# Kernel tuning notes

Measured on AMD Instinct MI355X. Metric: run time of the kernel, lower is better.

## Reference

```python
import jax, jax.numpy as jnp
import numpy as np

DIM = 1024
HEADS = 8
DK = 64
DV = 64
B = 4
N = 2048
SCALE = DK ** -0.5


def setup_inputs() -> dict:
    key = jax.random.key(0)
    ks = jax.random.split(key, 6)
    x = jax.random.normal(ks[0], (B, N, DIM), dtype=jnp.float32)
    # xavier-uniform-like init scale for weights (stored as [in, out], i.e. W^T of torch Linear weight)
    def xavier(k, fan_in, fan_out):
        limit = (6.0 / (fan_in + fan_out)) ** 0.5
        return jax.random.uniform(k, (fan_in, fan_out), minval=-limit, maxval=limit, dtype=jnp.float32)
    Wq = xavier(ks[1], DIM, HEADS * DK)
    Wk = xavier(ks[2], DIM, HEADS * DK)
    Wv = xavier(ks[3], DIM, HEADS * DV)
    Wo = xavier(ks[4], HEADS * DV, DIM)
    bo = jnp.zeros((DIM,), dtype=jnp.float32)
    return {"x": x, "Wq": Wq, "Wk": Wk, "Wv": Wv, "Wo": Wo, "bo": bo}


def reference(x, Wq, Wk, Wv, Wo, bo):
    b, n, _ = x.shape
    # project and split heads: b n (h d) -> b h n d
    def split_heads(t, d):
        return t.reshape(b, n, HEADS, d).transpose(0, 2, 1, 3)
    q = split_heads(x @ Wq, DK) * SCALE
    k = split_heads(x @ Wk, DK)
    v = split_heads(x @ Wv, DV)
    logits = jnp.einsum('bhid,bhjd->bhij', q, k)  # [b,h,n,n]
    attn = jax.nn.softmax(logits, axis=-1)
    out = jnp.einsum('bhij,bhjd->bhid', attn, v)  # [b,h,n,dv]
    out = out.transpose(0, 2, 1, 3).reshape(b, n, HEADS * DV)
    return (out @ Wo + bo, attn)
```

## Files before the change

### kernel.cpp

```cpp
#include <hip/hip_runtime.h>
#include <stdint.h>

#define B_ 4
#define N_ 2048
#define H_ 8
#define BH_ 32
#define DIM_ 1024

typedef unsigned short ushort_t;
typedef float f32x4 __attribute__((ext_vector_type(4)));
typedef short bf16x8 __attribute__((ext_vector_type(8)));

__device__ __forceinline__ ushort_t f2bf(float f) {
  uint32_t u = __float_as_uint(f);
  u += 0x7fff + ((u >> 16) & 1);
  return (ushort_t)(u >> 16);
}

__device__ __forceinline__ void lds_load16(const void* g, void* l) {
  __builtin_amdgcn_global_load_lds(
      (const __attribute__((address_space(1))) unsigned int*)g,
      (__attribute__((address_space(3))) unsigned int*)l, 16, 0, 0);
}

__global__ void cvt_x_kernel(const float* __restrict__ src, ushort_t* __restrict__ dst) {
  int i = (blockIdx.x * 256 + threadIdx.x) * 4;
  float4 v = *(const float4*)(src + i);
  ushort4 o;
  o.x = f2bf(v.x); o.y = f2bf(v.y); o.z = f2bf(v.z); o.w = f2bf(v.w);
  *(ushort4*)(dst + i) = o;
}

__global__ void twT_kernel(const float* __restrict__ src, ushort_t* __restrict__ dst,
                           int R, int C) {
  __shared__ float t[32][33];
  int c0 = blockIdx.x * 32, r0 = blockIdx.y * 32;
  int tx = threadIdx.x, ty = threadIdx.y;
#pragma unroll
  for (int i = 0; i < 4; i++)
    t[ty + i * 8][tx] = src[(size_t)(r0 + ty + i * 8) * C + c0 + tx];
  __syncthreads();
#pragma unroll
  for (int i = 0; i < 4; i++)
    dst[(size_t)(c0 + ty + i * 8) * R + r0 + tx] = f2bf(t[tx][ty + i * 8]);
}

__global__ void tv_kernel(const ushort_t* __restrict__ V, ushort_t* __restrict__ Vt) {
  __shared__ ushort_t t[64][65];
  int bh = blockIdx.y, n0 = blockIdx.x * 64;
  int tid = threadIdx.x;
  const ushort_t* Vh = V + (size_t)bh * N_ * 64;
  ushort_t* Vth = Vt + (size_t)bh * 64 * N_;
#pragma unroll
  for (int i = 0; i < 16; i++) {
    int idx = tid + i * 256;
    int r = idx >> 6, c = idx & 63;
    t[r][c] = Vh[(size_t)(n0 + r) * 64 + c];
  }
  __syncthreads();
#pragma unroll
  for (int i = 0; i < 16; i++) {
    int idx = tid + i * 256;
    int d = idx >> 6, c = idx & 63;
    Vth[(size_t)d * N_ + n0 + c] = t[c][d];
  }
}

template <int MODE>
__global__ __launch_bounds__(256)
void gemm_bf16_kernel(const ushort_t* __restrict__ A, const ushort_t* __restrict__ BT,
                      int K, int Ncols,
                      ushort_t* __restrict__ qb, ushort_t* __restrict__ kb2,
                      ushort_t* __restrict__ vb,
                      float* __restrict__ outp, const float* __restrict__ bias) {
  __shared__ ushort_t As[128 * 32];
  __shared__ ushort_t Bs[128 * 32];
  const int n0 = blockIdx.x * 128, m0 = blockIdx.y * 128;
  const int tid = threadIdx.x;
  const int lane = tid & 63, wave = tid >> 6;
  const int quad = lane >> 4, l16 = lane & 15;
  const int wm = (wave >> 1) * 64, wn = (wave & 1) * 64;
  f32x4 acc[4][4] = {};
  const int arow = tid >> 2, achk = tid & 3;
  const ushort_t* Ag = A + (size_t)(m0 + arow) * K + achk * 8;
  const ushort_t* Bg = BT + (size_t)(n0 + arow) * K + achk * 8;
  ushort_t* asd = As + tid * 8;
  ushort_t* bsd = Bs + tid * 8;
  const int nk = K >> 5;
  for (int ks = 0; ks < nk; ks++) {
    __syncthreads();
    lds_load16(Ag + ks * 32, asd);
    lds_load16(Ag + (size_t)64 * K + ks * 32, asd + 64 * 32);
    lds_load16(Bg + ks * 32, bsd);
    lds_load16(Bg + (size_t)64 * K + ks * 32, bsd + 64 * 32);
    __syncthreads();
    bf16x8 af[4], bfr[4];
#pragma unroll
    for (int i = 0; i < 4; i++)
      af[i] = *(const bf16x8*)(As + (wm + i * 16 + l16) * 32 + quad * 8);
#pragma unroll
    for (int i = 0; i < 4; i++)
      bfr[i] = *(const bf16x8*)(Bs + (wn + i * 16 + l16) * 32 + quad * 8);
#pragma unroll
    for (int i = 0; i < 4; i++)
#pragma unroll
      for (int j = 0; j < 4; j++)
        acc[i][j] = __builtin_amdgcn_mfma_f32_16x16x32_bf16(af[i], bfr[j], acc[i][j], 0, 0, 0);
  }
#pragma unroll
  for (int i = 0; i < 4; i++)
#pragma unroll
    for (int j = 0; j < 4; j++)
#pragma unroll
      for (int r = 0; r < 4; r++) {
        int gm = m0 + wm + i * 16 + quad * 4 + r;
        int gn = n0 + wn + j * 16 + l16;
        float v = acc[i][j][r];
        if (MODE == 0) {
          int b = gm >> 11, n = gm & (N_ - 1);
          int part = gn >> 9;
          int cc = gn & 511;
          int h = cc >> 6, d = cc & 63;
          size_t dst = ((size_t)(b * H_ + h) * N_ + n) * 64 + d;
          if (part == 0) qb[dst] = f2bf(v * 0.125f);
          else if (part == 1) kb2[dst] = f2bf(v);
          else vb[dst] = f2bf(v);
        } else {
          outp[(size_t)gm * Ncols + gn] = v + bias[gn];
        }
      }
}

#define PCOLS 1032
__global__ __launch_bounds__(512, 4)
void attn_kernel(const ushort_t* __restrict__ Q, const ushort_t* __restrict__ Kb,
                 const ushort_t* __restrict__ Vt, float* __restrict__ attn_out,
                 ushort_t* __restrict__ Ob) {
  __shared__ ushort_t Pl[16 * PCOLS];
  __shared__ float redA[8 * 16];
  __shared__ float redB[8 * 16];
  __shared__ float Ored[4 * 256];
  const int bh = blockIdx.y;
  const int q0 = blockIdx.x * 16;
  const int tid = threadIdx.x;
  const int w = tid >> 6, lane = tid & 63, quad = lane >> 4, l16 = lane & 15;

  const ushort_t* Qh = Q + (size_t)bh * N_ * 64;
  const ushort_t* Kh = Kb + (size_t)bh * N_ * 64;
  const ushort_t* Vh = Vt + (size_t)bh * 64 * N_;

  bf16x8 qf0 = *(const bf16x8*)(Qh + (size_t)(q0 + l16) * 64 + quad * 8);
  bf16x8 qf1 = *(const bf16x8*)(Qh + (size_t)(q0 + l16) * 64 + 32 + quad * 8);

  const int ncol0 = w * 256;
  f32x4 acc[16];
#pragma unroll
  for (int t = 0; t < 16; t++) {
    const ushort_t* kp = Kh + (size_t)(ncol0 + t * 16 + l16) * 64 + quad * 8;
    bf16x8 kf0 = *(const bf16x8*)kp;
    bf16x8 kf1 = *(const bf16x8*)(kp + 32);
    f32x4 z = {};
    z = __builtin_amdgcn_mfma_f32_16x16x32_bf16(qf0, kf0, z, 0, 0, 0);
    acc[t] = __builtin_amdgcn_mfma_f32_16x16x32_bf16(qf1, kf1, z, 0, 0, 0);
  }

  float mx[4];
#pragma unroll
  for (int r = 0; r < 4; r++) {
    float m = acc[0][r];
#pragma unroll
    for (int t = 1; t < 16; t++) m = fmaxf(m, acc[t][r]);
    for (int off = 1; off < 16; off <<= 1) m = fmaxf(m, __shfl_xor(m, off));
    mx[r] = m;
  }
  if (l16 == 0)
#pragma unroll
    for (int r = 0; r < 4; r++) redA[w * 16 + quad * 4 + r] = mx[r];
  __syncthreads();
#pragma unroll
  for (int r = 0; r < 4; r++) {
    float m = redA[quad * 4 + r];
#pragma unroll
    for (int ww = 1; ww < 8; ww++) m = fmaxf(m, redA[ww * 16 + quad * 4 + r]);
    mx[r] = m;
  }

  float sm[4] = {0.f, 0.f, 0.f, 0.f};
#pragma unroll
  for (int t = 0; t < 16; t++)
#pragma unroll
    for (int r = 0; r < 4; r++) {
      float p = __expf(acc[t][r] - mx[r]);
      acc[t][r] = p;
      sm[r] += p;
    }
#pragma unroll
  for (int r = 0; r < 4; r++) {
    float s = sm[r];
    for (int off = 1; off < 16; off <<= 1) s += __shfl_xor(s, off);
    sm[r] = s;
  }
  if (l16 == 0)
#pragma unroll
    for (int r = 0; r < 4; r++) redB[w * 16 + quad * 4 + r] = sm[r];
  __syncthreads();
  float inv[4];
#pragma unroll
  for (int r = 0; r < 4; r++) {
    float s = 0.f;
#pragma unroll
    for (int ww = 0; ww < 8; ww++) s += redB[ww * 16 + quad * 4 + r];
    inv[r] = 1.0f / s;
  }
#pragma unroll
  for (int t = 0; t < 16; t++)
#pragma unroll
    for (int r = 0; r < 4; r++) acc[t][r] *= inv[r];

  float* ar = attn_out + ((size_t)bh * N_ + q0) * N_;
#pragma unroll
  for (int t = 0; t < 16; t++) {
    int col = ncol0 + t * 16 + l16;
#pragma unroll
    for (int r = 0; r < 4; r++)
      ar[(size_t)(quad * 4 + r) * N_ + col] = acc[t][r];
  }

  const int jt = w & 3, kh = w >> 2;
  f32x4 oacc = {};
  for (int ph = 0; ph < 2; ph++) {
    if (kh == ph) {
#pragma unroll
      for (int t = 0; t < 16; t++) {
        int colb = jt * 256 + t * 16 + l16;
#pragma unroll
        for (int r = 0; r < 4; r++)
          Pl[(quad * 4 + r) * PCOLS + colb] = f2bf(acc[t][r]);
      }
    }
    __syncthreads();
#pragma unroll
    for (int s = 0; s < 16; s++) {
      int klocal = kh * 512 + s * 32;
      bf16x8 pf = *(const bf16x8*)(Pl + l16 * PCOLS + klocal + quad * 8);
      const ushort_t* vp = Vh + (size_t)(jt * 16 + l16) * N_ + ph * 1024 + klocal + quad * 8;
      bf16x8 vf = *(const bf16x8*)vp;
      oacc = __builtin_amdgcn_mfma_f32_16x16x32_bf16(pf, vf, oacc, 0, 0, 0);
    }
    __syncthreads();
  }
  if (w >= 4) {
#pragma unroll
    for (int r = 0; r < 4; r++)
      Ored[jt * 256 + (quad * 4 + r) * 16 + l16] = oacc[r];
  }
  __syncthreads();
  if (w < 4) {
    int b = bh >> 3, h = bh & 7;
#pragma unroll
    for (int r = 0; r < 4; r++) {
      float s = oacc[r] + Ored[jt * 256 + (quad * 4 + r) * 16 + l16];
      Ob[((size_t)(b * N_ + q0 + quad * 4 + r)) * 512 + h * 64 + jt * 16 + l16] = f2bf(s);
    }
  }
}

extern "C" void kernel_launch(void* const* d_in, const int* in_sizes, int n_in,
                              void* d_out, int out_size, void* d_ws, size_t ws_size,
                              hipStream_t stream) {
  const float* x  = (const float*)d_in[0];
  const float* Wq = (const float*)d_in[1];
  const float* Wk = (const float*)d_in[2];
  const float* Wv = (const float*)d_in[3];
  const float* Wo = (const float*)d_in[4];
  const float* bo = (const float*)d_in[5];
  float* outp = (float*)d_out;
  float* attnp = outp + (size_t)B_ * N_ * DIM_;

  char* ws = (char*)d_ws;
  ushort_t* xbf   = (ushort_t*)(ws);
  ushort_t* WallT = (ushort_t*)(ws + 16777216);
  ushort_t* WoT   = (ushort_t*)(ws + 19922944);
  ushort_t* Qb    = (ushort_t*)(ws + 20971520);
  ushort_t* Kb    = (ushort_t*)(ws + 29360128);
  ushort_t* Vb    = (ushort_t*)(ws + 37748736);
  ushort_t* Vt    = (ushort_t*)(ws + 46137344);
  ushort_t* Ob    = (ushort_t*)(ws + 54525952);

  cvt_x_kernel<<<dim3(8192), dim3(256), 0, stream>>>(x, xbf);
  twT_kernel<<<dim3(16, 32), dim3(32, 8), 0, stream>>>(Wq, WallT, 1024, 512);
  twT_kernel<<<dim3(16, 32), dim3(32, 8), 0, stream>>>(Wk, WallT + 512 * 1024, 1024, 512);
  twT_kernel<<<dim3(16, 32), dim3(32, 8), 0, stream>>>(Wv, WallT + 1024 * 1024, 1024, 512);
  twT_kernel<<<dim3(32, 16), dim3(32, 8), 0, stream>>>(Wo, WoT, 512, 1024);

  gemm_bf16_kernel<0><<<dim3(12, 64), dim3(256), 0, stream>>>(
      xbf, WallT, 1024, 1536, Qb, Kb, Vb, nullptr, nullptr);

  tv_kernel<<<dim3(32, 32), dim3(256), 0, stream>>>(Vb, Vt);

  attn_kernel<<<dim3(128, 32), dim3(512), 0, stream>>>(Qb, Kb, Vt, attnp, Ob);

  gemm_bf16_kernel<1><<<dim3(8, 64), dim3(256), 0, stream>>>(
      Ob, WoT, 512, 1024, nullptr, nullptr, nullptr, outp, bo);
}
```

Before: 875.5 us.

## Remap block order for XCD locality, merge weight transposes, use nontemporal stores

Flattens the grids of the projection GEMMs and the attention kernel and remaps block indices so that consecutive blocks landing on the same XCD (round-robin over 8) process neighbouring tiles or the same head. This improves L2 reuse of K/V and of the GEMM operands. The large fp32 attention-matrix store and the output-projection store become nontemporal, so the streaming writes pollute the cache less. The three QKV weight-transpose launches are merged into one 3D-grid launch to cut launch overhead.

```diff
diff --git a/kernel.cpp b/kernel.cpp
--- a/kernel.cpp
+++ b/kernel.cpp
@@ -43,6 +43,22 @@
 #pragma unroll
   for (int i = 0; i < 4; i++)
     dst[(size_t)(c0 + ty + i * 8) * R + r0 + tx] = f2bf(t[tx][ty + i * 8]);
+}
+
+__global__ void twT3_kernel(const float* __restrict__ Wq, const float* __restrict__ Wk,
+                            const float* __restrict__ Wv, ushort_t* __restrict__ dst) {
+  __shared__ float t[32][33];
+  const float* src = (blockIdx.z == 0) ? Wq : (blockIdx.z == 1) ? Wk : Wv;
+  ushort_t* d = dst + (size_t)blockIdx.z * 512 * 1024;
+  int c0 = blockIdx.x * 32, r0 = blockIdx.y * 32;
+  int tx = threadIdx.x, ty = threadIdx.y;
+#pragma unroll
+  for (int i = 0; i < 4; i++)
+    t[ty + i * 8][tx] = src[(size_t)(r0 + ty + i * 8) * 512 + c0 + tx];
+  __syncthreads();
+#pragma unroll
+  for (int i = 0; i < 4; i++)
+    d[(size_t)(c0 + ty + i * 8) * 1024 + r0 + tx] = f2bf(t[tx][ty + i * 8]);
 }
 
 __global__ void tv_kernel(const ushort_t* __restrict__ V, ushort_t* __restrict__ Vt) {
@@ -75,7 +91,12 @@
                       float* __restrict__ outp, const float* __restrict__ bias) {
   __shared__ ushort_t As[128 * 32];
   __shared__ ushort_t Bs[128 * 32];
-  const int n0 = blockIdx.x * 128, m0 = blockIdx.y * 128;
+  const int cpx = (int)gridDim.x >> 3;
+  const int flat = blockIdx.x;
+  const int orig = (flat & 7) * cpx + (flat >> 3);
+  const int nbx = (MODE == 0) ? 12 : 8;
+  const int bx = orig % nbx, by = orig / nbx;
+  const int n0 = bx * 128, m0 = by * 128;
   const int tid = threadIdx.x;
   const int lane = tid & 63, wave = tid >> 6;
   const int quad = lane >> 4, l16 = lane & 15;
@@ -126,7 +147,7 @@
           else if (part == 1) kb2[dst] = f2bf(v);
           else vb[dst] = f2bf(v);
         } else {
-          outp[(size_t)gm * Ncols + gn] = v + bias[gn];
+          __builtin_nontemporal_store(v + bias[gn], &outp[(size_t)gm * Ncols + gn]);
         }
       }
 }
@@ -140,8 +161,10 @@
   __shared__ float redA[8 * 16];
   __shared__ float redB[8 * 16];
   __shared__ float Ored[4 * 256];
-  const int bh = blockIdx.y;
-  const int q0 = blockIdx.x * 16;
+  const int flat = blockIdx.x;
+  const int orig = (flat & 7) * 512 + (flat >> 3);
+  const int bh = orig >> 7;
+  const int q0 = (orig & 127) * 16;
   const int tid = threadIdx.x;
   const int w = tid >> 6, lane = tid & 63, quad = lane >> 4, l16 = lane & 15;
 
@@ -223,7 +246,7 @@
     int col = ncol0 + t * 16 + l16;
 #pragma unroll
     for (int r = 0; r < 4; r++)
-      ar[(size_t)(quad * 4 + r) * N_ + col] = acc[t][r];
+      __builtin_nontemporal_store(acc[t][r], &ar[(size_t)(quad * 4 + r) * N_ + col]);
   }
 
   const int jt = w & 3, kh = w >> 2;
@@ -288,18 +311,16 @@
   ushort_t* Ob    = (ushort_t*)(ws + 54525952);
 
   cvt_x_kernel<<<dim3(8192), dim3(256), 0, stream>>>(x, xbf);
-  twT_kernel<<<dim3(16, 32), dim3(32, 8), 0, stream>>>(Wq, WallT, 1024, 512);
-  twT_kernel<<<dim3(16, 32), dim3(32, 8), 0, stream>>>(Wk, WallT + 512 * 1024, 1024, 512);
-  twT_kernel<<<dim3(16, 32), dim3(32, 8), 0, stream>>>(Wv, WallT + 1024 * 1024, 1024, 512);
+  twT3_kernel<<<dim3(16, 32, 3), dim3(32, 8), 0, stream>>>(Wq, Wk, Wv, WallT);
   twT_kernel<<<dim3(32, 16), dim3(32, 8), 0, stream>>>(Wo, WoT, 512, 1024);
 
-  gemm_bf16_kernel<0><<<dim3(12, 64), dim3(256), 0, stream>>>(
+  gemm_bf16_kernel<0><<<dim3(768), dim3(256), 0, stream>>>(
       xbf, WallT, 1024, 1536, Qb, Kb, Vb, nullptr, nullptr);
 
   tv_kernel<<<dim3(32, 32), dim3(256), 0, stream>>>(Vb, Vt);
 
-  attn_kernel<<<dim3(128, 32), dim3(512), 0, stream>>>(Qb, Kb, Vt, attnp, Ob);
-
-  gemm_bf16_kernel<1><<<dim3(8, 64), dim3(256), 0, stream>>>(
+  attn_kernel<<<dim3(4096), dim3(512), 0, stream>>>(Qb, Kb, Vt, attnp, Ob);
+
+  gemm_bf16_kernel<1><<<dim3(512), dim3(256), 0, stream>>>(
       Ob, WoT, 512, 1024, nullptr, nullptr, nullptr, outp, bo);
 }
```

Result: faster. 832.7 us (-4.9%).
